# Kernel optimization log

Measured on AMD Instinct MI355X. Metric: run time of the kernel, lower is better.

The kernel has to match this reference:

```python
import jax, jax.numpy as jnp
import numpy as np

C = 128          # channel_size
H = 2            # num_head
HD = C // H      # per-head dim = 64
SCALE = C ** 0.5 # note: module scales by sqrt(channel_size), not sqrt(head_dim)


def setup_inputs() -> dict:
    key = jax.random.key(0)
    k_x, k_w, k_b = jax.random.split(key, 3)
    x = jax.random.normal(k_x, (8, 64, 256, C), dtype=jnp.float32)
    # nn.Linear(C, 3C): weight [3C, C], bias [3C]; y = x @ W.T + b
    bound = 1.0 / np.sqrt(C)
    W_qkv = jax.random.uniform(k_w, (3 * C, C), dtype=jnp.float32, minval=-bound, maxval=bound)
    b_qkv = jax.random.uniform(k_b, (3 * C,), dtype=jnp.float32, minval=-bound, maxval=bound)
    return {"x": x, "W_qkv": W_qkv, "b_qkv": b_qkv}


def reference(x, W_qkv, b_qkv):
    b, l, g, _ = x.shape
    qkv = jnp.einsum('blgc,dc->blgd', x, W_qkv) + b_qkv        # [b,l,g,3C]
    # rearrange 'b l g (d h c) -> d b l h g c'
    qkv = qkv.reshape(b, l, g, 3, H, HD)
    qkv = jnp.transpose(qkv, (3, 0, 1, 4, 2, 5))               # [3,b,l,h,g,c]
    q, k, v = qkv[0], qkv[1], qkv[2]
    score = jnp.einsum('blhgc,blhkc->blhgk', q, k) / SCALE      # [b,l,h,g,g]
    score = jax.nn.softmax(score, axis=-1)
    out = jnp.einsum('blhgk,blhkc->blhgc', score, v)            # [b,l,h,g,c]
    # rearrange 'b l h g c -> b l g (h c)'
    out = jnp.transpose(out, (0, 1, 3, 2, 4)).reshape(b, l, g, H * HD)
    return out
```

## Files before the change

### kernel.cpp

```cpp
#include <hip/hip_runtime.h>
#include <hip/hip_bf16.h>


typedef __bf16 bf16x8 __attribute__((ext_vector_type(8)));
typedef float  f32x4  __attribute__((ext_vector_type(4)));

#define MFMA16(a, b, c) __builtin_amdgcn_mfma_f32_16x16x32_bf16((a), (b), (c), 0, 0, 0)

namespace dmsa {

constexpr int G  = 256;
constexpr int C  = 128;
constexpr int HD = 64;
constexpr float QSCALE = 1.4426950408889634f * 0.08838834764831845f;

__device__ __forceinline__ unsigned pack2(float a, float b) {
    union { __hip_bfloat162 h; unsigned u; } c;
    c.h = __float22bfloat162_rn(make_float2(a, b));
    return c.u;
}
__device__ __forceinline__ uint2 pack4(float a, float b, float c, float d) {
    uint2 r; r.x = pack2(a, b); r.y = pack2(c, d); return r;
}
__device__ __forceinline__ uint4 pack8(const float* p) {
    uint4 r;
    r.x = pack2(p[0], p[1]); r.y = pack2(p[2], p[3]);
    r.z = pack2(p[4], p[5]); r.w = pack2(p[6], p[7]);
    return r;
}
__device__ __forceinline__ bf16x8 lds8(const ushort* p) { return *(const bf16x8*)p; }
__device__ __forceinline__ bf16x8 ldg8(const ushort* p) { return *(const bf16x8*)p; }

__global__ void convw(const float* __restrict__ W, ushort* __restrict__ wbf) {
    int t = blockIdx.x * 256 + threadIdx.x;
    float tmp[8];
    const float* p = W + (size_t)t * 8;
    *(float4*)tmp       = *(const float4*)p;
    *(float4*)(tmp + 4) = *(const float4*)(p + 4);
    *(uint4*)(wbf + (size_t)t * 8) = pack8(tmp);
}

__global__ void convx(const float* __restrict__ x, ushort* __restrict__ xbf) {
    size_t t = (size_t)blockIdx.x * 256 + threadIdx.x;
    float tmp[8];
    const float* p = x + t * 8;
    *(float4*)tmp       = *(const float4*)p;
    *(float4*)(tmp + 4) = *(const float4*)(p + 4);
    *(uint4*)(xbf + t * 8) = pack8(tmp);
}

__global__ __launch_bounds__(256, 2)
void fused(const ushort* __restrict__ xb, const ushort* __restrict__ wb,
           const float* __restrict__ bias, float* __restrict__ out)
{
    __shared__ ushort kc[G * 72];
    __shared__ ushort vc[HD * 264];
    __shared__ ushort pt[4 * 32 * 40];

    const int tid = threadIdx.x, wv = tid >> 6, lane = tid & 63;
    const int l16 = lane & 15, quad = lane >> 4;

    const int b  = blockIdx.x;
    const int L  = ((b & 7) << 7) | (b >> 3);
    const int bl = L >> 1, h = L & 1;

    const ushort* xr = xb + (size_t)bl * G * C;
    const ushort* Wq = wb + (size_t)(h * HD) * C;
    const ushort* Wk = wb + (size_t)(C + h * HD) * C;
    const ushort* Wv = wb + (size_t)(2 * C + h * HD) * C;

    const int r0 = wv * 64;
    const f32x4 z4 = {0.f, 0.f, 0.f, 0.f};

    f32x4 qacc[4][4];
    #pragma unroll
    for (int mi = 0; mi < 4; ++mi)
        #pragma unroll
        for (int ni = 0; ni < 4; ++ni) qacc[mi][ni] = z4;

    #pragma unroll
    for (int kk = 0; kk < 4; ++kk) {
        bf16x8 bx[4];
        #pragma unroll
        for (int ni = 0; ni < 4; ++ni)
            bx[ni] = ldg8(xr + (size_t)(r0 + ni * 16 + l16) * C + kk * 32 + quad * 8);
        #pragma unroll
        for (int mi = 0; mi < 4; ++mi) {
            bf16x8 a = ldg8(Wq + (size_t)(mi * 16 + l16) * C + kk * 32 + quad * 8);
            #pragma unroll
            for (int ni = 0; ni < 4; ++ni)
                qacc[mi][ni] = MFMA16(a, bx[ni], qacc[mi][ni]);
        }
    }
    ushort* qs = kc + r0 * 72;
    #pragma unroll
    for (int mi = 0; mi < 4; ++mi) {
        float4 bs = *(const float4*)(bias + h * HD + mi * 16 + quad * 4);
        #pragma unroll
        for (int ni = 0; ni < 4; ++ni)
            *(uint2*)(qs + (ni * 16 + l16) * 72 + mi * 16 + quad * 4) =
                pack4((qacc[mi][ni][0] + bs.x) * QSCALE,
                      (qacc[mi][ni][1] + bs.y) * QSCALE,
                      (qacc[mi][ni][2] + bs.z) * QSCALE,
                      (qacc[mi][ni][3] + bs.w) * QSCALE);
    }
    bf16x8 qf[4][2];
    #pragma unroll
    for (int ni = 0; ni < 4; ++ni)
        #pragma unroll
        for (int kh = 0; kh < 2; ++kh)
            qf[ni][kh] = lds8(qs + (ni * 16 + l16) * 72 + kh * 32 + quad * 8);

    {
        f32x4 kacc[4][4];
        #pragma unroll
        for (int mi = 0; mi < 4; ++mi)
            #pragma unroll
            for (int nt = 0; nt < 4; ++nt) kacc[mi][nt] = z4;
        #pragma unroll
        for (int kk = 0; kk < 4; ++kk) {
            bf16x8 bx[4];
            #pragma unroll
            for (int nt = 0; nt < 4; ++nt)
                bx[nt] = ldg8(xr + (size_t)(r0 + nt * 16 + l16) * C + kk * 32 + quad * 8);
            #pragma unroll
            for (int mi = 0; mi < 4; ++mi) {
                bf16x8 a = ldg8(Wk + (size_t)(mi * 16 + l16) * C + kk * 32 + quad * 8);
                #pragma unroll
                for (int nt = 0; nt < 4; ++nt)
                    kacc[mi][nt] = MFMA16(a, bx[nt], kacc[mi][nt]);
            }
        }
        #pragma unroll
        for (int mi = 0; mi < 4; ++mi) {
            float4 bs = *(const float4*)(bias + C + h * HD + mi * 16 + quad * 4);
            #pragma unroll
            for (int nt = 0; nt < 4; ++nt)
                *(uint2*)(kc + (r0 + nt * 16 + l16) * 72 + mi * 16 + quad * 4) =
                    pack4(kacc[mi][nt][0] + bs.x, kacc[mi][nt][1] + bs.y,
                          kacc[mi][nt][2] + bs.z, kacc[mi][nt][3] + bs.w);
        }
    }

    {
        f32x4 vacc[4][4];
        #pragma unroll
        for (int mt = 0; mt < 4; ++mt)
            #pragma unroll
            for (int nt = 0; nt < 4; ++nt) vacc[mt][nt] = z4;
        #pragma unroll
        for (int kk = 0; kk < 4; ++kk) {
            bf16x8 ax[4];
            #pragma unroll
            for (int mt = 0; mt < 4; ++mt)
                ax[mt] = ldg8(xr + (size_t)(r0 + mt * 16 + l16) * C + kk * 32 + quad * 8);
            #pragma unroll
            for (int nt = 0; nt < 4; ++nt) {
                bf16x8 bw = ldg8(Wv + (size_t)(nt * 16 + l16) * C + kk * 32 + quad * 8);
                #pragma unroll
                for (int mt = 0; mt < 4; ++mt)
                    vacc[mt][nt] = MFMA16(ax[mt], bw, vacc[mt][nt]);
            }
        }
        #pragma unroll
        for (int nt = 0; nt < 4; ++nt) {
            float bv = bias[2 * C + h * HD + nt * 16 + l16];
            #pragma unroll
            for (int mt = 0; mt < 4; ++mt)
                *(uint2*)(vc + (nt * 16 + l16) * 264 + r0 + mt * 16 + quad * 4) =
                    pack4(vacc[mt][nt][0] + bv, vacc[mt][nt][1] + bv,
                          vacc[mt][nt][2] + bv, vacc[mt][nt][3] + bv);
        }
    }

    __syncthreads();

    ushort* ptw = pt + wv * (32 * 40);
    float lacc[4] = {0.f, 0.f, 0.f, 0.f};
    f32x4 oacc[4][4];
    #pragma unroll
    for (int mi = 0; mi < 4; ++mi)
        #pragma unroll
        for (int ni = 0; ni < 4; ++ni) oacc[mi][ni] = z4;

    #pragma unroll 2
    for (int sp = 0; sp < 8; ++sp) {
        const int g0 = sp * 32;

        bf16x8 kf[2][2];
        #pragma unroll
        for (int kh = 0; kh < 2; ++kh)
            #pragma unroll
            for (int mi = 0; mi < 2; ++mi)
                kf[kh][mi] = lds8(kc + (g0 + mi * 16 + l16) * 72 + kh * 32 + quad * 8);
        bf16x8 vf[4];
        #pragma unroll
        for (int mi = 0; mi < 4; ++mi)
            vf[mi] = lds8(vc + (mi * 16 + l16) * 264 + g0 + quad * 8);

        #pragma unroll
        for (int nig = 0; nig < 2; ++nig) {
            f32x4 s[2][2];
            #pragma unroll
            for (int mi = 0; mi < 2; ++mi)
                #pragma unroll
                for (int nj = 0; nj < 2; ++nj) s[mi][nj] = z4;
            __builtin_amdgcn_s_setprio(1);
            #pragma unroll
            for (int kh = 0; kh < 2; ++kh)
                #pragma unroll
                for (int mi = 0; mi < 2; ++mi)
                    #pragma unroll
                    for (int nj = 0; nj < 2; ++nj)
                        s[mi][nj] = MFMA16(kf[kh][mi], qf[nig * 2 + nj][kh], s[mi][nj]);
            __builtin_amdgcn_s_setprio(0);

            #pragma unroll
            for (int mi = 0; mi < 2; ++mi)
                #pragma unroll
                for (int nj = 0; nj < 2; ++nj) {
                    #pragma unroll
                    for (int r = 0; r < 4; ++r) {
                        float p = exp2f(s[mi][nj][r]);
                        s[mi][nj][r] = p;
                        lacc[nig * 2 + nj] += p;
                    }
                    *(uint2*)(ptw + (nj * 16 + l16) * 40 + mi * 16 + quad * 4) =
                        pack4(s[mi][nj][0], s[mi][nj][1], s[mi][nj][2], s[mi][nj][3]);
                }

            bf16x8 pf[2];
            #pragma unroll
            for (int nj = 0; nj < 2; ++nj)
                pf[nj] = lds8(ptw + (nj * 16 + l16) * 40 + quad * 8);
            __builtin_amdgcn_s_setprio(1);
            #pragma unroll
            for (int mi = 0; mi < 4; ++mi)
                #pragma unroll
                for (int nj = 0; nj < 2; ++nj)
                    oacc[mi][nig * 2 + nj] = MFMA16(vf[mi], pf[nj], oacc[mi][nig * 2 + nj]);
            __builtin_amdgcn_s_setprio(0);
        }
    }

    float* og = out + (size_t)bl * G * C + h * HD;
    #pragma unroll
    for (int ni = 0; ni < 4; ++ni) {
        float l = lacc[ni];
        l += __shfl_xor(l, 16);
        l += __shfl_xor(l, 32);
        float inv = 1.0f / l;
        int g = r0 + ni * 16 + l16;
        #pragma unroll
        for (int mi = 0; mi < 4; ++mi) {
            float4 st;
            st.x = oacc[mi][ni][0] * inv; st.y = oacc[mi][ni][1] * inv;
            st.z = oacc[mi][ni][2] * inv; st.w = oacc[mi][ni][3] * inv;
            *(float4*)(og + (size_t)g * C + mi * 16 + quad * 4) = st;
        }
    }
}

}

extern "C" void kernel_launch(void* const* d_in, const int* in_sizes, int n_in,
                              void* d_out, int out_size, void* d_ws, size_t ws_size,
                              hipStream_t stream) {
    (void)in_sizes; (void)n_in; (void)out_size;

    const size_t XBF = (size_t)512 * 256 * 128;
    if (ws_size < XBF * 2 + 384 * 128 * 2) return;

    const float* x    = (const float*)d_in[0];
    const float* W    = (const float*)d_in[1];
    const float* bias = (const float*)d_in[2];
    float* out = (float*)d_out;

    ushort* xbf = (ushort*)d_ws;
    ushort* wbf = xbf + XBF;

    dmsa::convw<<<dim3(24),   dim3(256), 0, stream>>>(W, wbf);
    dmsa::convx<<<dim3(8192), dim3(256), 0, stream>>>(x, xbf);
    dmsa::fused<<<dim3(1024), dim3(256), 0, stream>>>(xbf, wbf, bias, out);
}
```

Baseline: 177.7 us.

## Fuse x bf16 conversion into attention kernel and use 32x32 MFMA with permlane

Removes the standalone x-to-bf16 conversion kernel and instead loads fp32 x directly in the fused kernel, converting it once into registers that are reused for the Q, K and V projections. The attention loop switches to 32x32x16 MFMA tiles and moves the probability matrix between lanes with permlane32_swap instead of a shared-memory round trip. This cuts a full global write/read pass of x and some LDS traffic, at the cost of higher register pressure from holding x fragments and larger accumulators.

```diff
diff --git a/kernel.cpp b/kernel.cpp
--- a/kernel.cpp
+++ b/kernel.cpp
@@ -4,8 +4,10 @@
 
 typedef __bf16 bf16x8 __attribute__((ext_vector_type(8)));
 typedef float  f32x4  __attribute__((ext_vector_type(4)));
+typedef float  f32x16 __attribute__((ext_vector_type(16)));
 
 #define MFMA16(a, b, c) __builtin_amdgcn_mfma_f32_16x16x32_bf16((a), (b), (c), 0, 0, 0)
+#define MFMA32(a, b, c) __builtin_amdgcn_mfma_f32_32x32x16_bf16((a), (b), (c), 0, 0, 0)
 
 namespace dmsa {
 
@@ -30,6 +32,14 @@
 }
 __device__ __forceinline__ bf16x8 lds8(const ushort* p) { return *(const bf16x8*)p; }
 __device__ __forceinline__ bf16x8 ldg8(const ushort* p) { return *(const bf16x8*)p; }
+__device__ __forceinline__ bf16x8 ld8f(const float* __restrict__ p) {
+    float t[8];
+    *(float4*)t       = *(const float4*)p;
+    *(float4*)(t + 4) = *(const float4*)(p + 4);
+    union { uint4 u; bf16x8 v; } c;
+    c.u = pack8(t);
+    return c.v;
+}
 
 __global__ void convw(const float* __restrict__ W, ushort* __restrict__ wbf) {
     int t = blockIdx.x * 256 + threadIdx.x;
@@ -40,31 +50,22 @@
     *(uint4*)(wbf + (size_t)t * 8) = pack8(tmp);
 }
 
-__global__ void convx(const float* __restrict__ x, ushort* __restrict__ xbf) {
-    size_t t = (size_t)blockIdx.x * 256 + threadIdx.x;
-    float tmp[8];
-    const float* p = x + t * 8;
-    *(float4*)tmp       = *(const float4*)p;
-    *(float4*)(tmp + 4) = *(const float4*)(p + 4);
-    *(uint4*)(xbf + t * 8) = pack8(tmp);
-}
-
 __global__ __launch_bounds__(256, 2)
-void fused(const ushort* __restrict__ xb, const ushort* __restrict__ wb,
+void fused(const float* __restrict__ x, const ushort* __restrict__ wb,
            const float* __restrict__ bias, float* __restrict__ out)
 {
     __shared__ ushort kc[G * 72];
     __shared__ ushort vc[HD * 264];
-    __shared__ ushort pt[4 * 32 * 40];
 
     const int tid = threadIdx.x, wv = tid >> 6, lane = tid & 63;
     const int l16 = lane & 15, quad = lane >> 4;
+    const int l32 = lane & 31, hl = lane >> 5;
 
     const int b  = blockIdx.x;
     const int L  = ((b & 7) << 7) | (b >> 3);
     const int bl = L >> 1, h = L & 1;
 
-    const ushort* xr = xb + (size_t)bl * G * C;
+    const float*  xr = x  + (size_t)bl * G * C;
     const ushort* Wq = wb + (size_t)(h * HD) * C;
     const ushort* Wk = wb + (size_t)(C + h * HD) * C;
     const ushort* Wv = wb + (size_t)(2 * C + h * HD) * C;
@@ -72,26 +73,27 @@
     const int r0 = wv * 64;
     const f32x4 z4 = {0.f, 0.f, 0.f, 0.f};
 
+    bf16x8 xf[4][4];
+    #pragma unroll
+    for (int i = 0; i < 4; ++i)
+        #pragma unroll
+        for (int kk = 0; kk < 4; ++kk)
+            xf[i][kk] = ld8f(xr + (size_t)(r0 + i * 16 + l16) * C + kk * 32 + quad * 8);
+
     f32x4 qacc[4][4];
     #pragma unroll
     for (int mi = 0; mi < 4; ++mi)
         #pragma unroll
         for (int ni = 0; ni < 4; ++ni) qacc[mi][ni] = z4;
-
-    #pragma unroll
-    for (int kk = 0; kk < 4; ++kk) {
-        bf16x8 bx[4];
-        #pragma unroll
-        for (int ni = 0; ni < 4; ++ni)
-            bx[ni] = ldg8(xr + (size_t)(r0 + ni * 16 + l16) * C + kk * 32 + quad * 8);
+    #pragma unroll
+    for (int kk = 0; kk < 4; ++kk)
         #pragma unroll
         for (int mi = 0; mi < 4; ++mi) {
             bf16x8 a = ldg8(Wq + (size_t)(mi * 16 + l16) * C + kk * 32 + quad * 8);
             #pragma unroll
             for (int ni = 0; ni < 4; ++ni)
-                qacc[mi][ni] = MFMA16(a, bx[ni], qacc[mi][ni]);
-        }
-    }
+                qacc[mi][ni] = MFMA16(a, xf[ni][kk], qacc[mi][ni]);
+        }
     ushort* qs = kc + r0 * 72;
     #pragma unroll
     for (int mi = 0; mi < 4; ++mi) {
@@ -104,12 +106,12 @@
                       (qacc[mi][ni][2] + bs.z) * QSCALE,
                       (qacc[mi][ni][3] + bs.w) * QSCALE);
     }
-    bf16x8 qf[4][2];
-    #pragma unroll
-    for (int ni = 0; ni < 4; ++ni)
-        #pragma unroll
-        for (int kh = 0; kh < 2; ++kh)
-            qf[ni][kh] = lds8(qs + (ni * 16 + l16) * 72 + kh * 32 + quad * 8);
+    bf16x8 qf[2][4];
+    #pragma unroll
+    for (int ni = 0; ni < 2; ++ni)
+        #pragma unroll
+        for (int kk = 0; kk < 4; ++kk)
+            qf[ni][kk] = lds8(qs + (ni * 32 + l32) * 72 + kk * 16 + hl * 8);
 
     {
         f32x4 kacc[4][4];
@@ -118,19 +120,14 @@
             #pragma unroll
             for (int nt = 0; nt < 4; ++nt) kacc[mi][nt] = z4;
         #pragma unroll
-        for (int kk = 0; kk < 4; ++kk) {
-            bf16x8 bx[4];
-            #pragma unroll
-            for (int nt = 0; nt < 4; ++nt)
-                bx[nt] = ldg8(xr + (size_t)(r0 + nt * 16 + l16) * C + kk * 32 + quad * 8);
+        for (int kk = 0; kk < 4; ++kk)
             #pragma unroll
             for (int mi = 0; mi < 4; ++mi) {
                 bf16x8 a = ldg8(Wk + (size_t)(mi * 16 + l16) * C + kk * 32 + quad * 8);
                 #pragma unroll
                 for (int nt = 0; nt < 4; ++nt)
-                    kacc[mi][nt] = MFMA16(a, bx[nt], kacc[mi][nt]);
-            }
-        }
+                    kacc[mi][nt] = MFMA16(a, xf[nt][kk], kacc[mi][nt]);
+            }
         #pragma unroll
         for (int mi = 0; mi < 4; ++mi) {
             float4 bs = *(const float4*)(bias + C + h * HD + mi * 16 + quad * 4);
@@ -149,19 +146,14 @@
             #pragma unroll
             for (int nt = 0; nt < 4; ++nt) vacc[mt][nt] = z4;
         #pragma unroll
-        for (int kk = 0; kk < 4; ++kk) {
-            bf16x8 ax[4];
-            #pragma unroll
-            for (int mt = 0; mt < 4; ++mt)
-                ax[mt] = ldg8(xr + (size_t)(r0 + mt * 16 + l16) * C + kk * 32 + quad * 8);
+        for (int kk = 0; kk < 4; ++kk)
             #pragma unroll
             for (int nt = 0; nt < 4; ++nt) {
                 bf16x8 bw = ldg8(Wv + (size_t)(nt * 16 + l16) * C + kk * 32 + quad * 8);
                 #pragma unroll
                 for (int mt = 0; mt < 4; ++mt)
-                    vacc[mt][nt] = MFMA16(ax[mt], bw, vacc[mt][nt]);
-            }
-        }
+                    vacc[mt][nt] = MFMA16(xf[mt][kk], bw, vacc[mt][nt]);
+            }
         #pragma unroll
         for (int nt = 0; nt < 4; ++nt) {
             float bv = bias[2 * C + h * HD + nt * 16 + l16];
@@ -175,89 +167,88 @@
 
     __syncthreads();
 
-    ushort* ptw = pt + wv * (32 * 40);
-    float lacc[4] = {0.f, 0.f, 0.f, 0.f};
-    f32x4 oacc[4][4];
-    #pragma unroll
-    for (int mi = 0; mi < 4; ++mi)
-        #pragma unroll
-        for (int ni = 0; ni < 4; ++ni) oacc[mi][ni] = z4;
+    float lacc[2] = {0.f, 0.f};
+    f32x16 oacc[2][2];
+    #pragma unroll
+    for (int mt = 0; mt < 2; ++mt)
+        #pragma unroll
+        for (int ni = 0; ni < 2; ++ni)
+            #pragma unroll
+            for (int r = 0; r < 16; ++r) oacc[mt][ni][r] = 0.f;
 
     #pragma unroll 2
     for (int sp = 0; sp < 8; ++sp) {
         const int g0 = sp * 32;
 
-        bf16x8 kf[2][2];
-        #pragma unroll
-        for (int kh = 0; kh < 2; ++kh)
-            #pragma unroll
-            for (int mi = 0; mi < 2; ++mi)
-                kf[kh][mi] = lds8(kc + (g0 + mi * 16 + l16) * 72 + kh * 32 + quad * 8);
-        bf16x8 vf[4];
-        #pragma unroll
-        for (int mi = 0; mi < 4; ++mi)
-            vf[mi] = lds8(vc + (mi * 16 + l16) * 264 + g0 + quad * 8);
-
-        #pragma unroll
-        for (int nig = 0; nig < 2; ++nig) {
-            f32x4 s[2][2];
-            #pragma unroll
-            for (int mi = 0; mi < 2; ++mi)
+        bf16x8 kf[4];
+        #pragma unroll
+        for (int kk = 0; kk < 4; ++kk)
+            kf[kk] = lds8(kc + (g0 + l32) * 72 + kk * 16 + hl * 8);
+        bf16x8 vf[2][2];
+        #pragma unroll
+        for (int mt = 0; mt < 2; ++mt)
+            #pragma unroll
+            for (int ch = 0; ch < 2; ++ch)
+                vf[mt][ch] = lds8(vc + (mt * 32 + l32) * 264 + g0 + ch * 16 + hl * 8);
+
+        #pragma unroll
+        for (int ni = 0; ni < 2; ++ni) {
+            f32x16 s;
+            #pragma unroll
+            for (int r = 0; r < 16; ++r) s[r] = 0.f;
+            __builtin_amdgcn_s_setprio(1);
+            #pragma unroll
+            for (int kk = 0; kk < 4; ++kk)
+                s = MFMA32(kf[kk], qf[ni][kk], s);
+            __builtin_amdgcn_s_setprio(0);
+
+            float part = 0.f;
+            #pragma unroll
+            for (int r = 0; r < 16; ++r) {
+                float p = exp2f(s[r]);
+                s[r] = p;
+                part += p;
+            }
+            lacc[ni] += part;
+
+            #pragma unroll
+            for (int ch = 0; ch < 2; ++ch) {
+                unsigned p0a = pack2(s[8 * ch + 0], s[8 * ch + 1]);
+                unsigned p0b = pack2(s[8 * ch + 2], s[8 * ch + 3]);
+                unsigned p1a = pack2(s[8 * ch + 4], s[8 * ch + 5]);
+                unsigned p1b = pack2(s[8 * ch + 6], s[8 * ch + 7]);
+                auto w02 = __builtin_amdgcn_permlane32_swap((int)p0a, (int)p1a, false, false);
+                auto w13 = __builtin_amdgcn_permlane32_swap((int)p0b, (int)p1b, false, false);
+                union { uint4 u; bf16x8 v; } pf;
+                pf.u.x = (unsigned)w02[0]; pf.u.y = (unsigned)w13[0];
+                pf.u.z = (unsigned)w02[1]; pf.u.w = (unsigned)w13[1];
+                __builtin_amdgcn_s_setprio(1);
                 #pragma unroll
-                for (int nj = 0; nj < 2; ++nj) s[mi][nj] = z4;
-            __builtin_amdgcn_s_setprio(1);
-            #pragma unroll
-            for (int kh = 0; kh < 2; ++kh)
-                #pragma unroll
-                for (int mi = 0; mi < 2; ++mi)
-                    #pragma unroll
-                    for (int nj = 0; nj < 2; ++nj)
-                        s[mi][nj] = MFMA16(kf[kh][mi], qf[nig * 2 + nj][kh], s[mi][nj]);
-            __builtin_amdgcn_s_setprio(0);
-
-            #pragma unroll
-            for (int mi = 0; mi < 2; ++mi)
-                #pragma unroll
-                for (int nj = 0; nj < 2; ++nj) {
-                    #pragma unroll
-                    for (int r = 0; r < 4; ++r) {
-                        float p = exp2f(s[mi][nj][r]);
-                        s[mi][nj][r] = p;
-                        lacc[nig * 2 + nj] += p;
-                    }
-                    *(uint2*)(ptw + (nj * 16 + l16) * 40 + mi * 16 + quad * 4) =
-                        pack4(s[mi][nj][0], s[mi][nj][1], s[mi][nj][2], s[mi][nj][3]);
-                }
-
-            bf16x8 pf[2];
-            #pragma unroll
-            for (int nj = 0; nj < 2; ++nj)
-                pf[nj] = lds8(ptw + (nj * 16 + l16) * 40 + quad * 8);
-            __builtin_amdgcn_s_setprio(1);
-            #pragma unroll
-            for (int mi = 0; mi < 4; ++mi)
-                #pragma unroll
-                for (int nj = 0; nj < 2; ++nj)
-                    oacc[mi][nig * 2 + nj] = MFMA16(vf[mi], pf[nj], oacc[mi][nig * 2 + nj]);
-            __builtin_amdgcn_s_setprio(0);
+                for (int mt = 0; mt < 2; ++mt)
+                    oacc[mt][ni] = MFMA32(vf[mt][ch], pf.v, oacc[mt][ni]);
+                __builtin_amdgcn_s_setprio(0);
+            }
         }
     }
 
     float* og = out + (size_t)bl * G * C + h * HD;
     #pragma unroll
-    for (int ni = 0; ni < 4; ++ni) {
+    for (int ni = 0; ni < 2; ++ni) {
         float l = lacc[ni];
-        l += __shfl_xor(l, 16);
         l += __shfl_xor(l, 32);
         float inv = 1.0f / l;
-        int g = r0 + ni * 16 + l16;
-        #pragma unroll
-        for (int mi = 0; mi < 4; ++mi) {
-            float4 st;
-            st.x = oacc[mi][ni][0] * inv; st.y = oacc[mi][ni][1] * inv;
-            st.z = oacc[mi][ni][2] * inv; st.w = oacc[mi][ni][3] * inv;
-            *(float4*)(og + (size_t)g * C + mi * 16 + quad * 4) = st;
-        }
+        int g = r0 + ni * 32 + l32;
+        #pragma unroll
+        for (int mt = 0; mt < 2; ++mt)
+            #pragma unroll
+            for (int rr = 0; rr < 4; ++rr) {
+                float4 st;
+                st.x = oacc[mt][ni][4 * rr + 0] * inv;
+                st.y = oacc[mt][ni][4 * rr + 1] * inv;
+                st.z = oacc[mt][ni][4 * rr + 2] * inv;
+                st.w = oacc[mt][ni][4 * rr + 3] * inv;
+                *(float4*)(og + (size_t)g * C + mt * 32 + rr * 8 + hl * 4) = st;
+            }
     }
 }
 
@@ -268,18 +259,15 @@
                               hipStream_t stream) {
     (void)in_sizes; (void)n_in; (void)out_size;
 
-    const size_t XBF = (size_t)512 * 256 * 128;
-    if (ws_size < XBF * 2 + 384 * 128 * 2) return;
+    if (ws_size < (size_t)384 * 128 * 2) return;
 
     const float* x    = (const float*)d_in[0];
     const float* W    = (const float*)d_in[1];
     const float* bias = (const float*)d_in[2];
     float* out = (float*)d_out;
 
-    ushort* xbf = (ushort*)d_ws;
-    ushort* wbf = xbf + XBF;
+    ushort* wbf = (ushort*)d_ws;
 
     dmsa::convw<<<dim3(24),   dim3(256), 0, stream>>>(W, wbf);
-    dmsa::convx<<<dim3(8192), dim3(256), 0, stream>>>(x, xbf);
-    dmsa::fused<<<dim3(1024), dim3(256), 0, stream>>>(xbf, wbf, bias, out);
-}
+    dmsa::fused<<<dim3(1024), dim3(256), 0, stream>>>(x, wbf, bias, out);
+}
```

Result: faster. 166.1 us (-6.6%).
